# Optimization experiments

Hardware: AMD Instinct MI355X
Metric: run time of the kernel (lower is better)

## Reference

```python
import jax, jax.numpy as jnp
import numpy as np

EMBED_DIM = 2048
NUM_Q_HEADS = 16
HEAD_DIM = EMBED_DIM // NUM_Q_HEADS  # 128
SCALE = 1.0 / np.sqrt(EMBED_DIM)     # note: module uses 1/sqrt(embed_dim)
B, S = 4, 2048


def setup_inputs() -> dict:
    key = jax.random.key(0)
    ks = jax.random.split(key, 9)
    sd = 0.02
    return {
        "x": jax.random.normal(ks[0], (B, S, EMBED_DIM), dtype=jnp.float32),
        "Wq": jax.random.normal(ks[1], (EMBED_DIM, EMBED_DIM), dtype=jnp.float32) * sd,
        "bq": jnp.zeros((EMBED_DIM,), dtype=jnp.float32),
        "Wk": jax.random.normal(ks[2], (HEAD_DIM, EMBED_DIM), dtype=jnp.float32) * sd,
        "bk": jnp.zeros((HEAD_DIM,), dtype=jnp.float32),
        "Wv": jax.random.normal(ks[3], (HEAD_DIM, EMBED_DIM), dtype=jnp.float32) * sd,
        "bv": jnp.zeros((HEAD_DIM,), dtype=jnp.float32),
        "Wo": jax.random.normal(ks[4], (EMBED_DIM, EMBED_DIM), dtype=jnp.float32) * sd,
        "bo": jnp.zeros((EMBED_DIM,), dtype=jnp.float32),
    }


def reference(x, Wq, bq, Wk, bk, Wv, bv, Wo, bo):
    b, s, _ = x.shape
    # projections (nn.Linear: y = x @ W.T + b)
    q = (x @ Wq.T + bq).reshape(b, s, NUM_Q_HEADS, HEAD_DIM)  # [b,s,h,d]
    k = x @ Wk.T + bk   # [b,t,d] single KV head (MQA)
    v = x @ Wv.T + bv   # [b,t,d]
    # SDPA with single K/V head broadcast across all query heads
    scores = jnp.einsum("bshd,btd->bhst", q, k) * SCALE  # [b,h,s,t]
    attn = jax.nn.softmax(scores, axis=-1)
    out = jnp.einsum("bhst,btd->bshd", attn, v).reshape(b, s, EMBED_DIM)
    return out @ Wo.T + bo
```

## Files before the change

### kernel.cpp

```cpp
#include <hip/hip_runtime.h>
#include <stdint.h>
#include <cmath>

#define B_ 4
#define S_ 2048
#define E_ 2048
#define H_ 16
#define D_ 128
#define M_ (B_*S_)

typedef unsigned short u16;
typedef __attribute__((ext_vector_type(8))) short short8;
typedef __attribute__((ext_vector_type(4))) float f32x4;

__device__ __forceinline__ u16 f2bf(float f) {
  union { float f; uint32_t u; } v; v.f = f;
  uint32_t r = v.u + 0x7fffu + ((v.u >> 16) & 1u);
  return (u16)(r >> 16);
}

__device__ __forceinline__ float exp2_fast(float x) {
  float r; asm("v_exp_f32 %0, %1" : "=v"(r) : "v"(x)); return r;
}

__device__ __forceinline__ uint32_t cvtpk_bf16(float lo, float hi) {
  uint32_t r; asm("v_cvt_pk_bf16_f32 %0, %1, %2" : "=v"(r) : "v"(lo), "v"(hi));
  return r;
}

__device__ __forceinline__ void async16(const void* g, void* s) {
  __builtin_amdgcn_global_load_lds(
      (const __attribute__((address_space(1))) uint32_t*)g,
      (__attribute__((address_space(3))) uint32_t*)s, 16, 0, 0);
}

#define XSEG   4194304L
#define WQSEG  1048576L
#define WKSEG    65536L
__global__ __launch_bounds__(256) void cvt_all(
    const float4* __restrict__ x,  const float4* __restrict__ wq,
    const float4* __restrict__ wk, const float4* __restrict__ wv,
    const float4* __restrict__ wo,
    ushort4* __restrict__ xb,  ushort4* __restrict__ wqb,
    ushort4* __restrict__ wkb, ushort4* __restrict__ wvb,
    ushort4* __restrict__ wob) {
  long i = (long)blockIdx.x * 256 + threadIdx.x;
  const float4* src; ushort4* dst; long off;
  if (i < XSEG)                            { src = x;  dst = xb;  off = 0; }
  else if (i < XSEG + WQSEG)               { src = wq; dst = wqb; off = XSEG; }
  else if (i < XSEG + WQSEG + WKSEG)       { src = wk; dst = wkb; off = XSEG + WQSEG; }
  else if (i < XSEG + WQSEG + 2*WKSEG)     { src = wv; dst = wvb; off = XSEG + WQSEG + WKSEG; }
  else                                     { src = wo; dst = wob; off = XSEG + WQSEG + 2*WKSEG; }
  long j = i - off;
  float4 v = src[j];
  ushort4 o;
  o.x = f2bf(v.x); o.y = f2bf(v.y); o.z = f2bf(v.z); o.w = f2bf(v.w);
  dst[j] = o;
}

__global__ __launch_bounds__(256) void gemm_bt(
    const u16* __restrict__ A, const u16* __restrict__ Bm,
    const float* __restrict__ bias, float* __restrict__ Cout,
    int Mdim, int Ndim, int K, float oscale) {
  __shared__ u16 lA[128*64];
  __shared__ u16 lB[128*64];
  const int tid = threadIdx.x;
  const int l = tid & 63, w = tid >> 6;
  const int lr = l & 15, lg = l >> 4;
  const int wr = w >> 1, wc = w & 1;
  const int row0A = blockIdx.y * 128;
  const int row0B = blockIdx.x * 128;

  f32x4 acc[4][4] = {};

  for (int k0 = 0; k0 < K; k0 += 64) {
    __syncthreads();
    #pragma unroll
    for (int c = 0; c < 4; ++c) {
      int idx = c*256 + tid;
      int r = idx >> 3, ch = idx & 7;
      async16(A + (size_t)(row0A + r)*K + k0 + (ch ^ (r & 7))*8,
              lA + (size_t)(c*256 + w*64)*8);
    }
    #pragma unroll
    for (int c = 0; c < 4; ++c) {
      int idx = c*256 + tid;
      int r = idx >> 3, ch = idx & 7;
      async16(Bm + (size_t)(row0B + r)*K + k0 + (ch ^ (r & 7))*8,
              lB + (size_t)(c*256 + w*64)*8);
    }
    __syncthreads();
    #pragma unroll
    for (int ks = 0; ks < 2; ++ks) {
      short8 af[4], bfr[4];
      #pragma unroll
      for (int i = 0; i < 4; ++i) {
        int ra = wr*64 + i*16 + lr;
        af[i] = *(const short8*)((const char*)lA +
                 ((ra*128 + ks*64 + lg*16) ^ ((ra & 7) << 4)));
        int rb = wc*64 + i*16 + lr;
        bfr[i] = *(const short8*)((const char*)lB +
                 ((rb*128 + ks*64 + lg*16) ^ ((rb & 7) << 4)));
      }
      #pragma unroll
      for (int i = 0; i < 4; ++i)
        #pragma unroll
        for (int j = 0; j < 4; ++j)
          acc[i][j] = __builtin_amdgcn_mfma_f32_16x16x32_bf16(
                        af[i], bfr[j], acc[i][j], 0, 0, 0);
    }
  }

  const int crow0 = row0A + wr*64;
  const int ccol0 = row0B + wc*64;
  #pragma unroll
  for (int j = 0; j < 4; ++j) {
    int col = ccol0 + j*16 + lr;
    float bv = bias[col];
    #pragma unroll
    for (int i = 0; i < 4; ++i) {
      #pragma unroll
      for (int r = 0; r < 4; ++r) {
        int row = crow0 + i*16 + lg*4 + r;
        Cout[(size_t)row*Ndim + col] = (acc[i][j][r] + bv) * oscale;
      }
    }
  }
}

__global__ __launch_bounds__(256) void gemm_qkv(
    const u16* __restrict__ A, const u16* __restrict__ Wqb,
    const u16* __restrict__ Wkb, const u16* __restrict__ Wvb,
    const float* __restrict__ bq, const float* __restrict__ bk,
    const float* __restrict__ bv,
    u16* __restrict__ qb, u16* __restrict__ kb, u16* __restrict__ vTb,
    float qsc) {
  __shared__ u16 lA[128*64];
  __shared__ u16 lB[128*64];
  const int tid = threadIdx.x;
  const int l = tid & 63, w = tid >> 6;
  const int lr = l & 15, lg = l >> 4;
  const int wr = w >> 1, wc = w & 1;
  const int row0A = blockIdx.y * 128;
  const int bx = blockIdx.x;

  const u16* Bm; const float* bias; int mode; float osc = 1.0f;
  if (bx < 16)      { Bm = Wqb + (size_t)bx*128*E_; bias = bq + bx*128; mode = 0; osc = qsc; }
  else if (bx == 16){ Bm = Wkb; bias = bk; mode = 1; }
  else              { Bm = Wvb; bias = bv; mode = 2; }

  f32x4 acc[4][4] = {};

  for (int k0 = 0; k0 < E_; k0 += 64) {
    __syncthreads();
    #pragma unroll
    for (int c = 0; c < 4; ++c) {
      int idx = c*256 + tid;
      int r = idx >> 3, ch = idx & 7;
      async16(A + (size_t)(row0A + r)*E_ + k0 + (ch ^ (r & 7))*8,
              lA + (size_t)(c*256 + w*64)*8);
    }
    #pragma unroll
    for (int c = 0; c < 4; ++c) {
      int idx = c*256 + tid;
      int r = idx >> 3, ch = idx & 7;
      async16(Bm + (size_t)r*E_ + k0 + (ch ^ (r & 7))*8,
              lB + (size_t)(c*256 + w*64)*8);
    }
    __syncthreads();
    #pragma unroll
    for (int ks = 0; ks < 2; ++ks) {
      short8 af[4], bfr[4];
      #pragma unroll
      for (int i = 0; i < 4; ++i) {
        int ra = wr*64 + i*16 + lr;
        af[i] = *(const short8*)((const char*)lA +
                 ((ra*128 + ks*64 + lg*16) ^ ((ra & 7) << 4)));
        int rb = wc*64 + i*16 + lr;
        bfr[i] = *(const short8*)((const char*)lB +
                 ((rb*128 + ks*64 + lg*16) ^ ((rb & 7) << 4)));
      }
      #pragma unroll
      for (int i = 0; i < 4; ++i)
        #pragma unroll
        for (int j = 0; j < 4; ++j)
          acc[i][j] = __builtin_amdgcn_mfma_f32_16x16x32_bf16(
                        af[i], bfr[j], acc[i][j], 0, 0, 0);
    }
  }

  const int crow0 = row0A + wr*64;
  #pragma unroll
  for (int j = 0; j < 4; ++j) {
    int col = wc*64 + j*16 + lr;
    float bvv = bias[col];
    #pragma unroll
    for (int i = 0; i < 4; ++i) {
      #pragma unroll
      for (int r = 0; r < 4; ++r) {
        int row = crow0 + i*16 + lg*4 + r;
        float vo = (acc[i][j][r] + bvv) * osc;
        if (mode == 0)      qb[(size_t)row*E_ + bx*128 + col] = f2bf(vo);
        else if (mode == 1) kb[(size_t)row*D_ + col] = f2bf(vo);
        else                vTb[(size_t)col*M_ + row] = f2bf(vo);
      }
    }
  }
}

__global__ __launch_bounds__(512) void mqa_flash(
    const u16* __restrict__ q, const u16* __restrict__ k,
    const u16* __restrict__ vT, u16* __restrict__ o) {
  __shared__ u16 lKbuf[2][64*128];
  __shared__ u16 lVbuf[2][128*64];

  const int tid = threadIdx.x;
  const int l = tid & 63, w = tid >> 6;
  const int lr = l & 15, lg = l >> 4;
  const int qt = blockIdx.x, b = blockIdx.z;
  const int h = blockIdx.y*2 + (w >> 2);
  const int qrow0 = b*S_ + qt*128 + (w & 3)*32;

  short8 qf[2][4];
  #pragma unroll
  for (int st = 0; st < 2; ++st) {
    const u16* qp = q + (size_t)(qrow0 + st*16 + lr)*E_ + h*D_;
    #pragma unroll
    for (int ks = 0; ks < 4; ++ks)
      qf[st][ks] = *(const short8*)(qp + ks*32 + lg*8);
  }

  short8 ones;
  #pragma unroll
  for (int j = 0; j < 8; ++j) ones[j] = (short)0x3F80;

  f32x4 oa[2][8];
  f32x4 la[2] = {f32x4{0.f,0.f,0.f,0.f}, f32x4{0.f,0.f,0.f,0.f}};
  #pragma unroll
  for (int st = 0; st < 2; ++st)
    #pragma unroll
    for (int dn = 0; dn < 8; ++dn) oa[st][dn] = f32x4{0.f,0.f,0.f,0.f};

  const u16* kbase = k + (size_t)b*S_*D_;
  const u16* vbase = vT + (size_t)b*S_;
  char* lK0 = (char*)&lKbuf[0][0];
  char* lV0 = (char*)&lVbuf[0][0];

  auto STAGE = [&](int off, int tt) {
    #pragma unroll
    for (int c = 0; c < 2; ++c) {
      int idx = c*512 + tid;
      int s = idx >> 4, ch = idx & 15;
      int pr = (s & 32) | ((s & 12) << 1) | ((s & 16) >> 2) | (s & 3);
      async16(kbase + (size_t)(tt + pr)*D_ + (ch ^ (s & 7))*8,
              lK0 + off + (size_t)(c*512 + w*64)*16);
    }
    #pragma unroll
    for (int c = 0; c < 2; ++c) {
      int idx = c*512 + tid;
      int r = idx >> 3, ch = idx & 7;
      async16(vbase + (size_t)r*M_ + tt + (ch ^ (r & 7))*8,
              lV0 + off + (size_t)(c*512 + w*64)*16);
    }
  };

  STAGE(0, 0);
  __syncthreads();
  int roff = 0;

  for (int t0 = 0; t0 < S_; t0 += 64) {
    const int woff = roff ^ 16384;
    if (t0 + 64 < S_) STAGE(woff, t0 + 64);

    const char* lKc = lK0 + roff;
    const char* lVc = lV0 + roff;

    f32x4 sa[2][4];
    #pragma unroll
    for (int st = 0; st < 2; ++st)
      #pragma unroll
      for (int n = 0; n < 4; ++n) sa[st][n] = f32x4{0.f,0.f,0.f,0.f};
    __builtin_amdgcn_s_setprio(1);
    #pragma unroll
    for (int n = 0; n < 4; ++n)
      #pragma unroll
      for (int ks = 0; ks < 4; ++ks) {
        short8 kf = *(const short8*)(lKc +
                    (((n*16 + lr)*256 + ks*64 + lg*16) ^ ((lr & 7) << 4)));
        sa[0][n] = __builtin_amdgcn_mfma_f32_16x16x32_bf16(kf, qf[0][ks], sa[0][n], 0, 0, 0);
        sa[1][n] = __builtin_amdgcn_mfma_f32_16x16x32_bf16(kf, qf[1][ks], sa[1][n], 0, 0, 0);
      }
    __builtin_amdgcn_s_setprio(0);

    short8 pa[2][2];
    #pragma unroll
    for (int st = 0; st < 2; ++st) {
      #pragma unroll
      for (int n = 0; n < 4; ++n)
        #pragma unroll
        for (int r = 0; r < 4; ++r)
          sa[st][n][r] = exp2_fast(sa[st][n][r]);
      #pragma unroll
      for (int ks = 0; ks < 2; ++ks) {
        union { short8 s8; uint32_t u[4]; } pu;
        pu.u[0] = cvtpk_bf16(sa[st][2*ks  ][0], sa[st][2*ks  ][1]);
        pu.u[1] = cvtpk_bf16(sa[st][2*ks  ][2], sa[st][2*ks  ][3]);
        pu.u[2] = cvtpk_bf16(sa[st][2*ks+1][0], sa[st][2*ks+1][1]);
        pu.u[3] = cvtpk_bf16(sa[st][2*ks+1][2], sa[st][2*ks+1][3]);
        pa[st][ks] = pu.s8;
      }
    }

    __builtin_amdgcn_s_setprio(1);
    la[0] = __builtin_amdgcn_mfma_f32_16x16x32_bf16(pa[0][0], ones, la[0], 0, 0, 0);
    la[0] = __builtin_amdgcn_mfma_f32_16x16x32_bf16(pa[0][1], ones, la[0], 0, 0, 0);
    la[1] = __builtin_amdgcn_mfma_f32_16x16x32_bf16(pa[1][0], ones, la[1], 0, 0, 0);
    la[1] = __builtin_amdgcn_mfma_f32_16x16x32_bf16(pa[1][1], ones, la[1], 0, 0, 0);

    #pragma unroll
    for (int dn = 0; dn < 8; ++dn)
      #pragma unroll
      for (int ks = 0; ks < 2; ++ks) {
        short8 vf = *(const short8*)(lVc +
                    (((dn*16 + lr)*128 + ks*64 + lg*16) ^ ((lr & 7) << 4)));
        oa[0][dn] = __builtin_amdgcn_mfma_f32_16x16x32_bf16(pa[0][ks], vf, oa[0][dn], 0, 0, 0);
        oa[1][dn] = __builtin_amdgcn_mfma_f32_16x16x32_bf16(pa[1][ks], vf, oa[1][dn], 0, 0, 0);
      }
    __builtin_amdgcn_s_setprio(0);

    __syncthreads();
    roff = woff;
  }

  #pragma unroll
  for (int st = 0; st < 2; ++st) {
    #pragma unroll
    for (int r = 0; r < 4; ++r) {
      float inv = 1.0f / la[st][r];
      u16* orow = o + (size_t)(qrow0 + st*16 + lg*4 + r)*E_ + h*D_ + lr;
      #pragma unroll
      for (int dn = 0; dn < 8; ++dn)
        orow[dn*16] = f2bf(oa[st][dn][r] * inv);
    }
  }
}

extern "C" void kernel_launch(void* const* d_in, const int* in_sizes, int n_in,
                              void* d_out, int out_size, void* d_ws, size_t ws_size,
                              hipStream_t stream) {
  (void)in_sizes; (void)n_in; (void)out_size; (void)ws_size;
  const float* x  = (const float*)d_in[0];
  const float* Wq = (const float*)d_in[1];
  const float* bq = (const float*)d_in[2];
  const float* Wk = (const float*)d_in[3];
  const float* bk = (const float*)d_in[4];
  const float* Wv = (const float*)d_in[5];
  const float* bv = (const float*)d_in[6];
  const float* Wo = (const float*)d_in[7];
  const float* bo = (const float*)d_in[8];
  float* out = (float*)d_out;

  char* ws = (char*)d_ws;
  u16* xb  = (u16*)(ws + 0);
  u16* qb  = (u16*)(ws + 33554432);
  u16* kb  = (u16*)(ws + 67108864);
  u16* vbT = (u16*)(ws + 69206016);
  u16* Wqb = (u16*)(ws + 71303168);
  u16* Wkb = (u16*)(ws + 79691776);
  u16* Wvb = (u16*)(ws + 80216064);
  u16* Wob = (u16*)(ws + 80740352);
  u16* ob  = xb;

  cvt_all<<<25088, 256, 0, stream>>>(
      (const float4*)x, (const float4*)Wq, (const float4*)Wk,
      (const float4*)Wv, (const float4*)Wo,
      (ushort4*)xb, (ushort4*)Wqb, (ushort4*)Wkb, (ushort4*)Wvb, (ushort4*)Wob);

  float qsc = 1.44269504088896f / sqrtf((float)E_);
  gemm_qkv<<<dim3(18, M_/128), 256, 0, stream>>>(
      xb, Wqb, Wkb, Wvb, bq, bk, bv, qb, kb, vbT, qsc);

  mqa_flash<<<dim3(S_/128, H_/2, B_), 512, 0, stream>>>(qb, kb, vbT, ob);

  gemm_bt<<<dim3(E_/128, M_/128), 256, 0, stream>>>(ob, Wob, bo, out, M_, E_, E_, 1.0f);
}
```

Before: 367.4 us.

## Use double-buffered 256x256 tiled GEMM for Q and output projections

Replaces the 128x128 single-buffered GEMM kernels for the Q projection and the output projection with a 512-thread, 256x256-tile kernel. It double-buffers LDS with async loads issued two stages ahead, splits the MFMA work into phases, and raises wave priority around the MFMA phases. K and V projections move to a separate small kernel. The goal is more data reuse per tile and overlap of global loads with compute, at the cost of more LDS and registers per block, fewer blocks in the grid, and an extra launch.

Result: no change. 367.4 us (-0.0%).

```diff
diff --git a/kernel.cpp b/kernel.cpp
--- a/kernel.cpp
+++ b/kernel.cpp
@@ -58,10 +58,168 @@
   dst[j] = o;
 }
 
-__global__ __launch_bounds__(256) void gemm_bt(
+template<int OUT>
+__global__ __launch_bounds__(512, 2) void gemm256(
     const u16* __restrict__ A, const u16* __restrict__ Bm,
-    const float* __restrict__ bias, float* __restrict__ Cout,
-    int Mdim, int Ndim, int K, float oscale) {
+    const float* __restrict__ bias, void* __restrict__ Cout,
+    int Ndim, int K, float oscale) {
+  __shared__ u16 lA[2][256*64];
+  __shared__ u16 lB[2][256*64];
+  const int tid = threadIdx.x;
+  const int l = tid & 63, w = tid >> 6;
+  const int lr = l & 15, lg = l >> 4;
+  const int wm = w >> 2, wn = w & 3;
+  const int row0A = blockIdx.y * 256;
+  const int row0B = blockIdx.x * 256;
+
+  f32x4 acc[8][4] = {};
+
+  auto STAGE = [&](int d, int k0) {
+    #pragma unroll
+    for (int c = 0; c < 4; ++c) {
+      int idx = c*512 + tid;
+      int r = idx >> 3, ch = idx & 7;
+      async16(A + (size_t)(row0A + r)*K + k0 + (ch ^ (r & 7))*8,
+              &lA[d][(size_t)(c*512 + w*64)*8]);
+    }
+    #pragma unroll
+    for (int c = 0; c < 4; ++c) {
+      int idx = c*512 + tid;
+      int r = idx >> 3, ch = idx & 7;
+      async16(Bm + (size_t)(row0B + r)*K + k0 + (ch ^ (r & 7))*8,
+              &lB[d][(size_t)(c*512 + w*64)*8]);
+    }
+  };
+
+  STAGE(0, 0);
+  STAGE(1, 64);
+  asm volatile("s_waitcnt vmcnt(8)" ::: "memory");
+  __builtin_amdgcn_s_barrier();
+  asm volatile("" ::: "memory");
+
+  const int nk = K >> 6;
+  for (int k = 0; k < nk; ++k) {
+    const int d = k & 1;
+    const char* bA = (const char*)&lA[d][0];
+    const char* bB = (const char*)&lB[d][0];
+    short8 afr[8][2], bfr[4][2];
+
+    #pragma unroll
+    for (int i = 0; i < 4; ++i)
+      #pragma unroll
+      for (int ks = 0; ks < 2; ++ks) {
+        int ra = wm*128 + i*16 + lr;
+        afr[i][ks] = *(const short8*)(bA + ((ra*128 + ks*64 + lg*16) ^ ((ra & 7) << 4)));
+      }
+    #pragma unroll
+    for (int j = 0; j < 2; ++j)
+      #pragma unroll
+      for (int ks = 0; ks < 2; ++ks) {
+        int rb = wn*64 + j*16 + lr;
+        bfr[j][ks] = *(const short8*)(bB + ((rb*128 + ks*64 + lg*16) ^ ((rb & 7) << 4)));
+      }
+    __builtin_amdgcn_s_barrier();
+    asm volatile("" ::: "memory");
+    __builtin_amdgcn_s_setprio(1);
+    #pragma unroll
+    for (int i = 0; i < 4; ++i)
+      #pragma unroll
+      for (int j = 0; j < 2; ++j)
+        #pragma unroll
+        for (int ks = 0; ks < 2; ++ks)
+          acc[i][j] = __builtin_amdgcn_mfma_f32_16x16x32_bf16(
+                        afr[i][ks], bfr[j][ks], acc[i][j], 0, 0, 0);
+    __builtin_amdgcn_s_setprio(0);
+    __builtin_amdgcn_s_barrier();
+    asm volatile("" ::: "memory");
+
+    #pragma unroll
+    for (int j = 2; j < 4; ++j)
+      #pragma unroll
+      for (int ks = 0; ks < 2; ++ks) {
+        int rb = wn*64 + j*16 + lr;
+        bfr[j][ks] = *(const short8*)(bB + ((rb*128 + ks*64 + lg*16) ^ ((rb & 7) << 4)));
+      }
+    __builtin_amdgcn_s_barrier();
+    asm volatile("" ::: "memory");
+    __builtin_amdgcn_s_setprio(1);
+    #pragma unroll
+    for (int i = 0; i < 4; ++i)
+      #pragma unroll
+      for (int j = 2; j < 4; ++j)
+        #pragma unroll
+        for (int ks = 0; ks < 2; ++ks)
+          acc[i][j] = __builtin_amdgcn_mfma_f32_16x16x32_bf16(
+                        afr[i][ks], bfr[j][ks], acc[i][j], 0, 0, 0);
+    __builtin_amdgcn_s_setprio(0);
+    __builtin_amdgcn_s_barrier();
+    asm volatile("" ::: "memory");
+
+    #pragma unroll
+    for (int i = 4; i < 8; ++i)
+      #pragma unroll
+      for (int ks = 0; ks < 2; ++ks) {
+        int ra = wm*128 + i*16 + lr;
+        afr[i][ks] = *(const short8*)(bA + ((ra*128 + ks*64 + lg*16) ^ ((ra & 7) << 4)));
+      }
+    __builtin_amdgcn_s_barrier();
+    asm volatile("" ::: "memory");
+    __builtin_amdgcn_s_setprio(1);
+    #pragma unroll
+    for (int i = 4; i < 8; ++i)
+      #pragma unroll
+      for (int j = 0; j < 2; ++j)
+        #pragma unroll
+        for (int ks = 0; ks < 2; ++ks)
+          acc[i][j] = __builtin_amdgcn_mfma_f32_16x16x32_bf16(
+                        afr[i][ks], bfr[j][ks], acc[i][j], 0, 0, 0);
+    __builtin_amdgcn_s_setprio(0);
+    __builtin_amdgcn_s_barrier();
+    asm volatile("" ::: "memory");
+
+    bool st = (k + 2 < nk);
+    if (st) STAGE(d, (k + 2) << 6);
+    __builtin_amdgcn_s_barrier();
+    asm volatile("" ::: "memory");
+    __builtin_amdgcn_s_setprio(1);
+    #pragma unroll
+    for (int i = 4; i < 8; ++i)
+      #pragma unroll
+      for (int j = 2; j < 4; ++j)
+        #pragma unroll
+        for (int ks = 0; ks < 2; ++ks)
+          acc[i][j] = __builtin_amdgcn_mfma_f32_16x16x32_bf16(
+                        afr[i][ks], bfr[j][ks], acc[i][j], 0, 0, 0);
+    __builtin_amdgcn_s_setprio(0);
+    if (st) asm volatile("s_waitcnt vmcnt(8)" ::: "memory");
+    else    asm volatile("s_waitcnt vmcnt(0)" ::: "memory");
+    __builtin_amdgcn_s_barrier();
+    asm volatile("" ::: "memory");
+  }
+
+  const int crow0 = row0A + wm*128;
+  const int ccol0 = row0B + wn*64;
+  #pragma unroll
+  for (int j = 0; j < 4; ++j) {
+    int col = ccol0 + j*16 + lr;
+    float bv = bias[col];
+    #pragma unroll
+    for (int i = 0; i < 8; ++i) {
+      #pragma unroll
+      for (int r = 0; r < 4; ++r) {
+        int row = crow0 + i*16 + lg*4 + r;
+        float vo = (acc[i][j][r] + bv) * oscale;
+        if (OUT == 0) ((float*)Cout)[(size_t)row*Ndim + col] = vo;
+        else          ((u16*)Cout)[(size_t)row*Ndim + col] = f2bf(vo);
+      }
+    }
+  }
+}
+
+__global__ __launch_bounds__(256) void gemm_kv(
+    const u16* __restrict__ A, const u16* __restrict__ Wkb, const u16* __restrict__ Wvb,
+    const float* __restrict__ bkp, const float* __restrict__ bvp,
+    u16* __restrict__ kout, u16* __restrict__ vTout) {
   __shared__ u16 lA[128*64];
   __shared__ u16 lB[128*64];
   const int tid = threadIdx.x;
@@ -69,24 +227,26 @@
   const int lr = l & 15, lg = l >> 4;
   const int wr = w >> 1, wc = w & 1;
   const int row0A = blockIdx.y * 128;
-  const int row0B = blockIdx.x * 128;
+  const bool isV = (blockIdx.x != 0);
+  const u16* Bm = isV ? Wvb : Wkb;
+  const float* bias = isV ? bvp : bkp;
 
   f32x4 acc[4][4] = {};
 
-  for (int k0 = 0; k0 < K; k0 += 64) {
+  for (int k0 = 0; k0 < E_; k0 += 64) {
     __syncthreads();
     #pragma unroll
     for (int c = 0; c < 4; ++c) {
       int idx = c*256 + tid;
       int r = idx >> 3, ch = idx & 7;
-      async16(A + (size_t)(row0A + r)*K + k0 + (ch ^ (r & 7))*8,
+      async16(A + (size_t)(row0A + r)*E_ + k0 + (ch ^ (r & 7))*8,
               lA + (size_t)(c*256 + w*64)*8);
     }
     #pragma unroll
     for (int c = 0; c < 4; ++c) {
       int idx = c*256 + tid;
       int r = idx >> 3, ch = idx & 7;
-      async16(Bm + (size_t)(row0B + r)*K + k0 + (ch ^ (r & 7))*8,
+      async16(Bm + (size_t)r*E_ + k0 + (ch ^ (r & 7))*8,
               lB + (size_t)(c*256 + w*64)*8);
     }
     __syncthreads();
@@ -112,84 +272,6 @@
   }
 
   const int crow0 = row0A + wr*64;
-  const int ccol0 = row0B + wc*64;
-  #pragma unroll
-  for (int j = 0; j < 4; ++j) {
-    int col = ccol0 + j*16 + lr;
-    float bv = bias[col];
-    #pragma unroll
-    for (int i = 0; i < 4; ++i) {
-      #pragma unroll
-      for (int r = 0; r < 4; ++r) {
-        int row = crow0 + i*16 + lg*4 + r;
-        Cout[(size_t)row*Ndim + col] = (acc[i][j][r] + bv) * oscale;
-      }
-    }
-  }
-}
-
-__global__ __launch_bounds__(256) void gemm_qkv(
-    const u16* __restrict__ A, const u16* __restrict__ Wqb,
-    const u16* __restrict__ Wkb, const u16* __restrict__ Wvb,
-    const float* __restrict__ bq, const float* __restrict__ bk,
-    const float* __restrict__ bv,
-    u16* __restrict__ qb, u16* __restrict__ kb, u16* __restrict__ vTb,
-    float qsc) {
-  __shared__ u16 lA[128*64];
-  __shared__ u16 lB[128*64];
-  const int tid = threadIdx.x;
-  const int l = tid & 63, w = tid >> 6;
-  const int lr = l & 15, lg = l >> 4;
-  const int wr = w >> 1, wc = w & 1;
-  const int row0A = blockIdx.y * 128;
-  const int bx = blockIdx.x;
-
-  const u16* Bm; const float* bias; int mode; float osc = 1.0f;
-  if (bx < 16)      { Bm = Wqb + (size_t)bx*128*E_; bias = bq + bx*128; mode = 0; osc = qsc; }
-  else if (bx == 16){ Bm = Wkb; bias = bk; mode = 1; }
-  else              { Bm = Wvb; bias = bv; mode = 2; }
-
-  f32x4 acc[4][4] = {};
-
-  for (int k0 = 0; k0 < E_; k0 += 64) {
-    __syncthreads();
-    #pragma unroll
-    for (int c = 0; c < 4; ++c) {
-      int idx = c*256 + tid;
-      int r = idx >> 3, ch = idx & 7;
-      async16(A + (size_t)(row0A + r)*E_ + k0 + (ch ^ (r & 7))*8,
-              lA + (size_t)(c*256 + w*64)*8);
-    }
-    #pragma unroll
-    for (int c = 0; c < 4; ++c) {
-      int idx = c*256 + tid;
-      int r = idx >> 3, ch = idx & 7;
-      async16(Bm + (size_t)r*E_ + k0 + (ch ^ (r & 7))*8,
-              lB + (size_t)(c*256 + w*64)*8);
-    }
-    __syncthreads();
-    #pragma unroll
-    for (int ks = 0; ks < 2; ++ks) {
-      short8 af[4], bfr[4];
-      #pragma unroll
-      for (int i = 0; i < 4; ++i) {
-        int ra = wr*64 + i*16 + lr;
-        af[i] = *(const short8*)((const char*)lA +
-                 ((ra*128 + ks*64 + lg*16) ^ ((ra & 7) << 4)));
-        int rb = wc*64 + i*16 + lr;
-        bfr[i] = *(const short8*)((const char*)lB +
-                 ((rb*128 + ks*64 + lg*16) ^ ((rb & 7) << 4)));
-      }
-      #pragma unroll
-      for (int i = 0; i < 4; ++i)
-        #pragma unroll
-        for (int j = 0; j < 4; ++j)
-          acc[i][j] = __builtin_amdgcn_mfma_f32_16x16x32_bf16(
-                        af[i], bfr[j], acc[i][j], 0, 0, 0);
-    }
-  }
-
-  const int crow0 = row0A + wr*64;
   #pragma unroll
   for (int j = 0; j < 4; ++j) {
     int col = wc*64 + j*16 + lr;
@@ -199,10 +281,9 @@
       #pragma unroll
       for (int r = 0; r < 4; ++r) {
         int row = crow0 + i*16 + lg*4 + r;
-        float vo = (acc[i][j][r] + bvv) * osc;
-        if (mode == 0)      qb[(size_t)row*E_ + bx*128 + col] = f2bf(vo);
-        else if (mode == 1) kb[(size_t)row*D_ + col] = f2bf(vo);
-        else                vTb[(size_t)col*M_ + row] = f2bf(vo);
+        float vo = acc[i][j][r] + bvv;
+        if (isV) vTout[(size_t)col*M_ + row] = f2bf(vo);
+        else     kout[(size_t)row*D_ + col] = f2bf(vo);
       }
     }
   }
@@ -376,11 +457,12 @@
       (const float4*)Wv, (const float4*)Wo,
       (ushort4*)xb, (ushort4*)Wqb, (ushort4*)Wkb, (ushort4*)Wvb, (ushort4*)Wob);
 
+  gemm_kv<<<dim3(2, M_/128), 256, 0, stream>>>(xb, Wkb, Wvb, bk, bv, kb, vbT);
+
   float qsc = 1.44269504088896f / sqrtf((float)E_);
-  gemm_qkv<<<dim3(18, M_/128), 256, 0, stream>>>(
-      xb, Wqb, Wkb, Wvb, bq, bk, bv, qb, kb, vbT, qsc);
+  gemm256<1><<<dim3(E_/256, M_/256), 512, 0, stream>>>(xb, Wqb, bq, qb, E_, E_, qsc);
 
   mqa_flash<<<dim3(S_/128, H_/2, B_), 512, 0, stream>>>(qb, kb, vbT, ob);
 
-  gemm_bt<<<dim3(E_/128, M_/128), 256, 0, stream>>>(ob, Wob, bo, out, M_, E_, E_, 1.0f);
-}
+  gemm256<0><<<dim3(E_/256, M_/256), 512, 0, stream>>>(ob, Wob, bo, out, E_, E_, 1.0f);
+}
```
